# Performance work log

Hardware: AMD Instinct MI355X
Metric: run time of the kernel (lower is better)

## Reference

```python
import jax, jax.numpy as jnp
import numpy as np

IN_SIZE = 256
OUT_SIZE = 256
SCALE = 1.5


def compute_bboxes(bboxes_raw, scale):
    # mirrors CropFace._compute_bboxes: sort corner pairs, scale around center, clamp
    b = bboxes_raw.reshape(-1, 2, 2)          # [N, 2(points), 2(x,y)]
    b = jnp.sort(b, axis=-2)                  # per-coordinate sort -> (min pt, max pt)
    c = jnp.mean(b, axis=-2, keepdims=True)
    b = (b - c) * scale + c
    bmin = jnp.maximum(b[:, 0], 0.0)          # bboxes[:,0][<0]=0
    bmax = jnp.minimum(b[:, 1], 1.0)          # bboxes[:,1][>1]=1
    return jnp.concatenate([bmin, bmax], axis=-1)  # [N, 4] = x1,y1,x2,y2


def _crop_resize_one(img, box, S, H, W):
    # img: [3,H,W]; box: [4] normalized x1,y1,x2,y2
    # pixel bbox, truncation matches .long() on non-negative values
    xmin = (box[0] * W).astype(jnp.int32)
    ymin = (box[1] * H).astype(jnp.int32)
    xmax = (box[2] * W).astype(jnp.int32)
    ymax = (box[3] * H).astype(jnp.int32)
    wci = jnp.maximum(xmax - xmin, 1)  # guard degenerate crop
    hci = jnp.maximum(ymax - ymin, 1)
    wc = wci.astype(img.dtype)
    hc = hci.astype(img.dtype)
    i = jnp.arange(S, dtype=img.dtype)
    # bilinear resize source coords (align_corners=False convention)
    ys = jnp.clip(ymin + (i + 0.5) * hc / S - 0.5, ymin, ymin + hc - 1)
    xs = jnp.clip(xmin + (i + 0.5) * wc / S - 0.5, xmin, xmin + wc - 1)
    y0 = jnp.floor(ys).astype(jnp.int32)
    x0 = jnp.floor(xs).astype(jnp.int32)
    y1 = jnp.minimum(y0 + 1, ymin + hci - 1)
    x1 = jnp.minimum(x0 + 1, xmin + wci - 1)
    wy = (ys - y0)[:, None]   # [S,1]
    wx = (xs - x0)[None, :]   # [1,S]
    g = lambda yi, xi: img[:, yi[:, None], xi[None, :]]  # [3,S,S]
    out = ((1 - wy) * (1 - wx) * g(y0, x0)
           + (1 - wy) * wx * g(y0, x1)
           + wy * (1 - wx) * g(y1, x0)
           + wy * wx * g(y1, x1))
    return out


def crop_faces(imgs, bboxes_raw, has_face, out_size, scale):
    N, C, H, W = imgs.shape
    boxes = compute_bboxes(bboxes_raw, scale)
    cropped = jax.vmap(_crop_resize_one, in_axes=(0, 0, None, None, None))(
        imgs, boxes, out_size, H, W)                       # [N,3,S,S]
    face = (has_face[:, None, None, None] == 1)
    return jnp.where(face, cropped, jnp.zeros((), imgs.dtype))


def setup_inputs() -> dict:
    key = jax.random.key(0)
    k1, k2, k3 = jax.random.split(key, 3)
    imgs = jax.random.uniform(k1, (32, 3, 512, 512), dtype=jnp.float32)
    bboxes_raw = jax.random.uniform(k2, (32, 4), dtype=jnp.float32)
    has_face = jax.random.randint(k3, (32,), 0, 2, dtype=jnp.int32)
    return {"imgs": imgs, "bboxes_raw": bboxes_raw, "has_face": has_face}


def reference(imgs, bboxes_raw, has_face):
    return crop_faces(imgs, bboxes_raw, has_face, OUT_SIZE, SCALE)
```

## Files before the change

kernel.cpp:

```cpp
#include <hip/hip_runtime.h>

#define S 256
#define HH 512
#define WW 512

typedef float f2 __attribute__((ext_vector_type(2), aligned(4)));

__global__ __launch_bounds__(256) void cropface_kernel(
    const float* __restrict__ imgs,
    const float* __restrict__ bboxes,
    const int* __restrict__ has_face,
    float* __restrict__ out)
{
#pragma clang fp contract(off)
    int nwg = gridDim.x;
    int q = nwg >> 3, r = nwg & 7;
    int xcd = blockIdx.x & 7, idx = blockIdx.x >> 3;
    int w = (xcd < r ? xcd * (q + 1) : r * (q + 1) + (xcd - r) * q) + idx;

    int n = w >> 7;
    int ybase = (w & 127) << 1;
    int x = threadIdx.x;

    float* o0 = out + (size_t)(n * 3) * S * S + ybase * S + x;

    if (has_face[n] != 1) {
#pragma unroll
        for (int ch = 0; ch < 3; ++ch) {
            __builtin_nontemporal_store(0.0f, o0 + ch * S * S);
            __builtin_nontemporal_store(0.0f, o0 + ch * S * S + S);
        }
        return;
    }

    float bx0 = bboxes[4 * n + 0], by0 = bboxes[4 * n + 1];
    float bx1 = bboxes[4 * n + 2], by1 = bboxes[4 * n + 3];
    float xmn = fminf(bx0, bx1), xmx = fmaxf(bx0, bx1);
    float ymn = fminf(by0, by1), ymx = fmaxf(by0, by1);
    float cx = (xmn + xmx) * 0.5f;
    float cy = (ymn + ymx) * 0.5f;
    float sxmn = (xmn - cx) * 1.5f; sxmn = sxmn + cx;
    float sxmx = (xmx - cx) * 1.5f; sxmx = sxmx + cx;
    float symn = (ymn - cy) * 1.5f; symn = symn + cy;
    float symx = (ymx - cy) * 1.5f; symx = symx + cy;
    float b0 = fmaxf(sxmn, 0.0f);
    float b1 = fmaxf(symn, 0.0f);
    float b2 = fminf(sxmx, 1.0f);
    float b3 = fminf(symx, 1.0f);

    int xmin = (int)(b0 * 512.0f);
    int ymin = (int)(b1 * 512.0f);
    int xmax = (int)(b2 * 512.0f);
    int ymax = (int)(b3 * 512.0f);
    int wci = max(xmax - xmin, 1);
    int hci = max(ymax - ymin, 1);
    float wc = (float)wci, hc = (float)hci;

    float xs = (float)xmin + ((float)x + 0.5f) * wc / 256.0f - 0.5f;
    xs = fminf(fmaxf(xs, (float)xmin), (float)xmin + wc - 1.0f);
    int x0 = (int)xs;
    float wx = xs - (float)x0;
    float omwx = 1.0f - wx;
    int pbase = min(x0, 510);
    bool hi = (x0 > 510);

    int y0v[2], y1v[2];
    float wyv[2];
#pragma unroll
    for (int rr = 0; rr < 2; ++rr) {
        float ys = (float)ymin + ((float)(ybase + rr) + 0.5f) * hc / 256.0f - 0.5f;
        ys = fminf(fmaxf(ys, (float)ymin), (float)ymin + hc - 1.0f);
        int y0 = (int)ys;
        y0v[rr] = y0;
        y1v[rr] = min(y0 + 1, 511);
        wyv[rr] = ys - (float)y0;
    }

    const float* base = imgs + (size_t)n * 3 * HH * WW;
#pragma unroll
    for (int ch = 0; ch < 3; ++ch) {
        const float* p = base + (size_t)ch * HH * WW;
        f2 a0[2], a1[2];
#pragma unroll
        for (int rr = 0; rr < 2; ++rr) {
            a0[rr] = *(const f2*)(p + (size_t)y0v[rr] * WW + pbase);
            a1[rr] = *(const f2*)(p + (size_t)y1v[rr] * WW + pbase);
        }
#pragma unroll
        for (int rr = 0; rr < 2; ++rr) {
            float g00 = hi ? a0[rr].y : a0[rr].x;
            float g01 = a0[rr].y;
            float g10 = hi ? a1[rr].y : a1[rr].x;
            float g11 = a1[rr].y;
            float wy = wyv[rr];
            float omwy = 1.0f - wy;
            float acc = (omwy * omwx) * g00;
            acc = acc + (omwy * wx) * g01;
            acc = acc + (wy * omwx) * g10;
            acc = acc + (wy * wx) * g11;
            __builtin_nontemporal_store(acc, o0 + ch * S * S + rr * S);
        }
    }
}

extern "C" void kernel_launch(void* const* d_in, const int* in_sizes, int n_in,
                              void* d_out, int out_size, void* d_ws, size_t ws_size,
                              hipStream_t stream) {
    const float* imgs     = (const float*)d_in[0];
    const float* bboxes   = (const float*)d_in[1];
    const int*   has_face = (const int*)d_in[2];
    float* out = (float*)d_out;
    int N = in_sizes[2];
    int grid = N * 128;
    cropface_kernel<<<grid, 256, 0, stream>>>(imgs, bboxes, has_face, out);
}
```

Measured before the change: 12.60 us.

## Compute two adjacent output pixels per thread using 4-wide loads and tent weights

Each thread now produces two horizontally adjacent output pixels. It loads a 4-float window per source row and computes the two x-interpolations as dot products with tent-function weights. The grid is halved so each block covers 4 rows, and stores become 8-byte vector stores. Floating-point contraction is now allowed outside the bbox computation, so rounding may differ slightly from the reference. The tent weights assume the two samples fall within 4 pixels of pbase; that holds only when the scale factor wc/256 is small enough, and large crops could exceed the window.

```diff
diff --git a/kernel.cpp b/kernel.cpp
--- a/kernel.cpp
+++ b/kernel.cpp
@@ -4,7 +4,8 @@
 #define HH 512
 #define WW 512
 
-typedef float f2 __attribute__((ext_vector_type(2), aligned(4)));
+typedef float f4 __attribute__((ext_vector_type(4), aligned(4)));
+typedef float f2 __attribute__((ext_vector_type(2), aligned(8)));
 
 __global__ __launch_bounds__(256) void cropface_kernel(
     const float* __restrict__ imgs,
@@ -12,64 +13,82 @@
     const int* __restrict__ has_face,
     float* __restrict__ out)
 {
-#pragma clang fp contract(off)
     int nwg = gridDim.x;
     int q = nwg >> 3, r = nwg & 7;
     int xcd = blockIdx.x & 7, idx = blockIdx.x >> 3;
     int w = (xcd < r ? xcd * (q + 1) : r * (q + 1) + (xcd - r) * q) + idx;
 
-    int n = w >> 7;
-    int ybase = (w & 127) << 1;
-    int x = threadIdx.x;
+    int n = w >> 6;
+    int rowg = (w & 63) << 2;
+    int t = threadIdx.x;
+    int tx = t & 127;
+    int ty = t >> 7;
+    int ybase = rowg + (ty << 1);
+    int xg = tx << 1;
 
-    float* o0 = out + (size_t)(n * 3) * S * S + ybase * S + x;
+    float* o0 = out + (size_t)(n * 3) * S * S + ybase * S + xg;
 
     if (has_face[n] != 1) {
+        f2 z; z.x = 0.0f; z.y = 0.0f;
 #pragma unroll
         for (int ch = 0; ch < 3; ++ch) {
-            __builtin_nontemporal_store(0.0f, o0 + ch * S * S);
-            __builtin_nontemporal_store(0.0f, o0 + ch * S * S + S);
+            __builtin_nontemporal_store(z, (f2*)(o0 + ch * S * S));
+            __builtin_nontemporal_store(z, (f2*)(o0 + ch * S * S + S));
         }
         return;
     }
 
-    float bx0 = bboxes[4 * n + 0], by0 = bboxes[4 * n + 1];
-    float bx1 = bboxes[4 * n + 2], by1 = bboxes[4 * n + 3];
-    float xmn = fminf(bx0, bx1), xmx = fmaxf(bx0, bx1);
-    float ymn = fminf(by0, by1), ymx = fmaxf(by0, by1);
-    float cx = (xmn + xmx) * 0.5f;
-    float cy = (ymn + ymx) * 0.5f;
-    float sxmn = (xmn - cx) * 1.5f; sxmn = sxmn + cx;
-    float sxmx = (xmx - cx) * 1.5f; sxmx = sxmx + cx;
-    float symn = (ymn - cy) * 1.5f; symn = symn + cy;
-    float symx = (ymx - cy) * 1.5f; symx = symx + cy;
-    float b0 = fmaxf(sxmn, 0.0f);
-    float b1 = fmaxf(symn, 0.0f);
-    float b2 = fminf(sxmx, 1.0f);
-    float b3 = fminf(symx, 1.0f);
+    int xmin, ymin, wci, hci;
+    float wc, hc;
+    {
+#pragma clang fp contract(off)
+        float bx0 = bboxes[4 * n + 0], by0 = bboxes[4 * n + 1];
+        float bx1 = bboxes[4 * n + 2], by1 = bboxes[4 * n + 3];
+        float xmn = fminf(bx0, bx1), xmx = fmaxf(bx0, bx1);
+        float ymn = fminf(by0, by1), ymx = fmaxf(by0, by1);
+        float cx = (xmn + xmx) * 0.5f;
+        float cy = (ymn + ymx) * 0.5f;
+        float sxmn = (xmn - cx) * 1.5f; sxmn = sxmn + cx;
+        float sxmx = (xmx - cx) * 1.5f; sxmx = sxmx + cx;
+        float symn = (ymn - cy) * 1.5f; symn = symn + cy;
+        float symx = (ymx - cy) * 1.5f; symx = symx + cy;
+        float b0 = fmaxf(sxmn, 0.0f);
+        float b1 = fmaxf(symn, 0.0f);
+        float b2 = fminf(sxmx, 1.0f);
+        float b3 = fminf(symx, 1.0f);
+        xmin = (int)(b0 * 512.0f);
+        ymin = (int)(b1 * 512.0f);
+        int xmax = (int)(b2 * 512.0f);
+        int ymax = (int)(b3 * 512.0f);
+        wci = max(xmax - xmin, 1);
+        hci = max(ymax - ymin, 1);
+        wc = (float)wci;
+        hc = (float)hci;
+    }
 
-    int xmin = (int)(b0 * 512.0f);
-    int ymin = (int)(b1 * 512.0f);
-    int xmax = (int)(b2 * 512.0f);
-    int ymax = (int)(b3 * 512.0f);
-    int wci = max(xmax - xmin, 1);
-    int hci = max(ymax - ymin, 1);
-    float wc = (float)wci, hc = (float)hci;
+    float xlo = (float)xmin, xhi = (float)xmin + wc - 1.0f;
+    float xs0 = (float)xmin + ((float)xg + 0.5f) * wc / 256.0f - 0.5f;
+    xs0 = fminf(fmaxf(xs0, xlo), xhi);
+    float xs1 = (float)xmin + ((float)(xg + 1) + 0.5f) * wc / 256.0f - 0.5f;
+    xs1 = fminf(fmaxf(xs1, xlo), xhi);
+    int pbase = min((int)xs0, 508);
+    float pb = (float)pbase;
+    float xi0 = xs0 - pb;
+    float xi1 = xs1 - pb;
+    f4 wv0, wv1;
+#pragma unroll
+    for (int k = 0; k < 4; ++k) {
+        wv0[k] = fmaxf(0.0f, 1.0f - fabsf(xi0 - (float)k));
+        wv1[k] = fmaxf(0.0f, 1.0f - fabsf(xi1 - (float)k));
+    }
 
-    float xs = (float)xmin + ((float)x + 0.5f) * wc / 256.0f - 0.5f;
-    xs = fminf(fmaxf(xs, (float)xmin), (float)xmin + wc - 1.0f);
-    int x0 = (int)xs;
-    float wx = xs - (float)x0;
-    float omwx = 1.0f - wx;
-    int pbase = min(x0, 510);
-    bool hi = (x0 > 510);
-
+    float ylo = (float)ymin, yhic = (float)ymin + hc - 1.0f;
     int y0v[2], y1v[2];
     float wyv[2];
 #pragma unroll
     for (int rr = 0; rr < 2; ++rr) {
         float ys = (float)ymin + ((float)(ybase + rr) + 0.5f) * hc / 256.0f - 0.5f;
-        ys = fminf(fmaxf(ys, (float)ymin), (float)ymin + hc - 1.0f);
+        ys = fminf(fmaxf(ys, ylo), yhic);
         int y0 = (int)ys;
         y0v[rr] = y0;
         y1v[rr] = min(y0 + 1, 511);
@@ -80,25 +99,23 @@
 #pragma unroll
     for (int ch = 0; ch < 3; ++ch) {
         const float* p = base + (size_t)ch * HH * WW;
-        f2 a0[2], a1[2];
+        f4 va[2], vb[2];
 #pragma unroll
         for (int rr = 0; rr < 2; ++rr) {
-            a0[rr] = *(const f2*)(p + (size_t)y0v[rr] * WW + pbase);
-            a1[rr] = *(const f2*)(p + (size_t)y1v[rr] * WW + pbase);
+            va[rr] = *(const f4*)(p + (size_t)y0v[rr] * WW + pbase);
+            vb[rr] = *(const f4*)(p + (size_t)y1v[rr] * WW + pbase);
         }
 #pragma unroll
         for (int rr = 0; rr < 2; ++rr) {
-            float g00 = hi ? a0[rr].y : a0[rr].x;
-            float g01 = a0[rr].y;
-            float g10 = hi ? a1[rr].y : a1[rr].x;
-            float g11 = a1[rr].y;
-            float wy = wyv[rr];
-            float omwy = 1.0f - wy;
-            float acc = (omwy * omwx) * g00;
-            acc = acc + (omwy * wx) * g01;
-            acc = acc + (wy * omwx) * g10;
-            acc = acc + (wy * wx) * g11;
-            __builtin_nontemporal_store(acc, o0 + ch * S * S + rr * S);
+            float d00 = ((va[rr].x * wv0.x + va[rr].y * wv0.y) + va[rr].z * wv0.z) + va[rr].w * wv0.w;
+            float d01 = ((va[rr].x * wv1.x + va[rr].y * wv1.y) + va[rr].z * wv1.z) + va[rr].w * wv1.w;
+            float d10 = ((vb[rr].x * wv0.x + vb[rr].y * wv0.y) + vb[rr].z * wv0.z) + vb[rr].w * wv0.w;
+            float d11 = ((vb[rr].x * wv1.x + vb[rr].y * wv1.y) + vb[rr].z * wv1.z) + vb[rr].w * wv1.w;
+            float wy = wyv[rr], omwy = 1.0f - wy;
+            f2 st;
+            st.x = omwy * d00 + wy * d10;
+            st.y = omwy * d01 + wy * d11;
+            __builtin_nontemporal_store(st, (f2*)(o0 + ch * S * S + rr * S));
         }
     }
 }
@@ -111,6 +128,6 @@
     const int*   has_face = (const int*)d_in[2];
     float* out = (float*)d_out;
     int N = in_sizes[2];
-    int grid = N * 128;
+    int grid = N * 64;
     cropface_kernel<<<grid, 256, 0, stream>>>(imgs, bboxes, has_face, out);
 }
```

New measurement: 11.14 us. -11.5%, faster.
